# Performance work log

Hardware: AMD Instinct MI355X
Metric: run time of the kernel (lower is better)

## Reference

```python
import jax, jax.numpy as jnp
import numpy as np

B = 131072

def _lin(x, w, b):
    return x @ w.T + b

def setup_inputs() -> dict:
    key = jax.random.key(0)
    ks = jax.random.split(key, 32)
    def rn(k, shape, scale=0.05):
        return jax.random.normal(k, shape, dtype=jnp.float32) * scale
    inp = {
        "x": rn(ks[0], (B, 256), 1.0),
        "w": rn(ks[1], (B, 36), 1.0),
        "h0": rn(ks[2], (B, 32), 1.0),
        "c0": rn(ks[3], (B, 32), 1.0),
        "fc1_w": rn(ks[4], (128, 256)), "fc1_b": rn(ks[5], (128,)),
        "fc1a_w": rn(ks[6], (128, 164)), "fc1a_b": rn(ks[7], (128,)),
        "fc1b_w": rn(ks[8], (128, 128)), "fc1b_b": rn(ks[9], (128,)),
        "w_game": rn(ks[10], (1, 12), 1.0),
        "fc1c_w": rn(ks[11], (64, 140)), "fc1c_b": rn(ks[12], (64,)),
        "fc2_w": rn(ks[13], (32, 64)), "fc2_b": rn(ks[14], (32,)),
        "fc3_w": rn(ks[15], (32, 32)), "fc3_b": rn(ks[16], (32,)),
        "w_ih": rn(ks[17], (128, 32)), "w_hh": rn(ks[18], (128, 32)),
        "b_ih": rn(ks[19], (128,)), "b_hh": rn(ks[20], (128,)),
        "fc4_w": rn(ks[21], (32, 32)), "fc4_b": rn(ks[22], (32,)),
        "fc5_w": rn(ks[23], (1, 32)), "fc5_b": rn(ks[24], (1,)),
    }
    return inp

def reference(x, w, h0, c0, fc1_w, fc1_b, fc1a_w, fc1a_b, fc1b_w, fc1b_b,
              w_game, fc1c_w, fc1c_b, fc2_w, fc2_b, fc3_w, fc3_b,
              w_ih, w_hh, b_ih, b_hh, fc4_w, fc4_b, fc5_w, fc5_b):
    b = x.shape[0]
    h = jax.nn.relu(_lin(x, fc1_w, fc1_b))                      # [B,128]
    h = jnp.concatenate([h, w], axis=-1)                        # [B,164]
    h = jax.nn.relu(_lin(h, fc1a_w, fc1a_b))                    # [B,128]
    h = jax.nn.relu(_lin(h, fc1b_w, fc1b_b))                    # [B,128]
    wg = jnp.broadcast_to(w_game.reshape(1, 12), (b, 12))
    h = jnp.concatenate([h, wg], axis=-1)                       # [B,140]
    h = jax.nn.relu(_lin(h, fc1c_w, fc1c_b))                    # [B,64]
    h = jax.nn.relu(_lin(h, fc2_w, fc2_b))                      # [B,32]
    h = jax.nn.relu(_lin(h, fc3_w, fc3_b))                      # [B,32]
    # LSTMCell step (torch gate order: input, forget, cell, output)
    gates = _lin(h, w_ih, b_ih) + _lin(h0, w_hh, b_hh)          # [B,128]
    i_g, f_g, g_g, o_g = jnp.split(gates, 4, axis=-1)
    c_new = jax.nn.sigmoid(f_g) * c0 + jax.nn.sigmoid(i_g) * jnp.tanh(g_g)
    h_new = jax.nn.sigmoid(o_g) * jnp.tanh(c_new)               # [B,32]
    out = jax.nn.relu(_lin(h_new, fc4_w, fc4_b))                # [B,32]
    out = _lin(out, fc5_w, fc5_b)                               # [B,1]
    return jax.nn.sigmoid(out)
```

## Files before the change

kernel.cpp:

```cpp
#include <hip/hip_runtime.h>
#include <hip/hip_bf16.h>


typedef __bf16 bf16x8 __attribute__((ext_vector_type(8)));
typedef float  f32x4  __attribute__((ext_vector_type(4)));
typedef int    i32x4  __attribute__((ext_vector_type(4)));

#define MFMA16(A, B, C) __builtin_amdgcn_mfma_f32_16x16x32_bf16((A), (B), (C), 0, 0, 0)

#define WOFF_FC1A_H 0
#define WOFF_FC1B   16384
#define WOFF_FC1C   32768
#define LDS_ELEMS   40960
#define WOFF_FC1    40960
#define WOFF_FC1A_W 73728
#define WOFF_FC2    81920
#define WOFF_FC3    83968
#define WOFF_WIH    84992
#define WOFF_WHH    89088
#define WOFF_FC4    93184
#define WTOT        94208
#define BOFF_FC1  0
#define BOFF_FC1A 128
#define BOFF_FC1B 256
#define BOFF_FC1C 384
#define BOFF_FC2  448
#define BOFF_FC3  480
#define BOFF_LSTM 512
#define BOFF_FC4  640
#define BTOT      672

__device__ __forceinline__ void conv_frag(int rel, const float* __restrict__ src,
                                          __bf16* __restrict__ dst,
                                          int ns, int Krow, int kbase, int klim, int perm) {
    int j    = rel & 7;
    int lane = (rel >> 3) & 63;
    int fs   = rel >> 9;
    int s    = fs % ns;
    int t    = fs / ns;
    int gq   = lane >> 4;
    int n    = 16 * t + (lane & 15);
    int k    = perm ? (16 * (2 * s + (j >> 2)) + 4 * gq + (j & 3))
                    : (32 * s + 8 * gq + j);
    float v  = (k < klim) ? src[n * Krow + kbase + k] : 0.f;
    dst[rel] = (__bf16)v;
}

__global__ void prep_kernel(const float* __restrict__ fc1w,  const float* __restrict__ fc1b,
                            const float* __restrict__ fc1aw, const float* __restrict__ fc1ab,
                            const float* __restrict__ fc1bw, const float* __restrict__ fc1bb,
                            const float* __restrict__ wgame, const float* __restrict__ fc1cw,
                            const float* __restrict__ fc1cb, const float* __restrict__ fc2w,
                            const float* __restrict__ fc2b,  const float* __restrict__ fc3w,
                            const float* __restrict__ fc3b,  const float* __restrict__ wih,
                            const float* __restrict__ whh,   const float* __restrict__ bih,
                            const float* __restrict__ bhh,   const float* __restrict__ fc4w,
                            const float* __restrict__ fc4b,
                            __bf16* __restrict__ wsw, float* __restrict__ wsb) {
    int idx = blockIdx.x * 256 + threadIdx.x;
    if (idx < WTOT) {
        if      (idx < WOFF_FC1B)   conv_frag(idx - WOFF_FC1A_H, fc1aw, wsw + WOFF_FC1A_H, 4, 164,   0, 128, 1);
        else if (idx < WOFF_FC1C)   conv_frag(idx - WOFF_FC1B,   fc1bw, wsw + WOFF_FC1B,   4, 128,   0, 128, 1);
        else if (idx < WOFF_FC1)    conv_frag(idx - WOFF_FC1C,   fc1cw, wsw + WOFF_FC1C,   4, 140,   0, 128, 1);
        else if (idx < WOFF_FC1A_W) conv_frag(idx - WOFF_FC1,    fc1w,  wsw + WOFF_FC1,    8, 256,   0, 256, 0);
        else if (idx < WOFF_FC2)    conv_frag(idx - WOFF_FC1A_W, fc1aw, wsw + WOFF_FC1A_W, 2, 164, 128,  36, 0);
        else if (idx < WOFF_FC3)    conv_frag(idx - WOFF_FC2,    fc2w,  wsw + WOFF_FC2,    2,  64,   0,  64, 1);
        else if (idx < WOFF_WIH)    conv_frag(idx - WOFF_FC3,    fc3w,  wsw + WOFF_FC3,    1,  32,   0,  32, 1);
        else if (idx < WOFF_WHH)    conv_frag(idx - WOFF_WIH,    wih,   wsw + WOFF_WIH,    1,  32,   0,  32, 1);
        else if (idx < WOFF_FC4)    conv_frag(idx - WOFF_WHH,    whh,   wsw + WOFF_WHH,    1,  32,   0,  32, 0);
        else                        conv_frag(idx - WOFF_FC4,    fc4w,  wsw + WOFF_FC4,    1,  32,   0,  32, 1);
    } else if (idx < WTOT + BTOT) {
        int bi = idx - WTOT;
        float v;
        if      (bi < 128) v = fc1b[bi];
        else if (bi < 256) v = fc1ab[bi - 128];
        else if (bi < 384) v = fc1bb[bi - 256];
        else if (bi < 448) {
            int n = bi - 384;
            v = fc1cb[n];
            for (int q = 0; q < 12; ++q) v += fc1cw[n * 140 + 128 + q] * wgame[q];
        }
        else if (bi < 480) v = fc2b[bi - 448];
        else if (bi < 512) v = fc3b[bi - 480];
        else if (bi < 640) { int n = bi - 512; v = bih[n] + bhh[n]; }
        else               v = fc4b[bi - 640];
        wsb[bi] = v;
    }
}

__device__ __forceinline__ bf16x8 ld8f(const float* __restrict__ p) {
    f32x4 a = *(const f32x4*)p;
    f32x4 b = *(const f32x4*)(p + 4);
    bf16x8 r;
    r[0] = (__bf16)a[0]; r[1] = (__bf16)a[1]; r[2] = (__bf16)a[2]; r[3] = (__bf16)a[3];
    r[4] = (__bf16)b[0]; r[5] = (__bf16)b[1]; r[6] = (__bf16)b[2]; r[7] = (__bf16)b[3];
    return r;
}

__device__ __forceinline__ bf16x8 ld4f_masked(const float* __restrict__ p, bool on) {
    f32x4 v = {0.f, 0.f, 0.f, 0.f};
    if (on) v = *(const f32x4*)p;
    bf16x8 r;
    r[0] = (__bf16)v[0]; r[1] = (__bf16)v[1]; r[2] = (__bf16)v[2]; r[3] = (__bf16)v[3];
    r[4] = (__bf16)0.f;  r[5] = (__bf16)0.f;  r[6] = (__bf16)0.f;  r[7] = (__bf16)0.f;
    return r;
}

__device__ __forceinline__ bf16x8 packrelu(const f32x4* a, int s) {
    bf16x8 r;
#pragma unroll
    for (int j = 0; j < 8; ++j) {
        float v = a[2 * s + (j >> 2)][j & 3];
        r[j] = (__bf16)fmaxf(v, 0.f);
    }
    return r;
}

__device__ __forceinline__ float sigm(float v)  { return 1.f / (1.f + __expf(-v)); }
__device__ __forceinline__ float tanh_(float v) { return 1.f - 2.f / (1.f + __expf(2.f * v)); }

__global__ __launch_bounds__(512, 4) void fused_mlp_lstm(
        const float* __restrict__ x,  const float* __restrict__ w,
        const float* __restrict__ h0, const float* __restrict__ c0,
        const float* __restrict__ fc5w, const float* __restrict__ fc5b,
        const __bf16* __restrict__ wsw, const float* __restrict__ wsb,
        float* __restrict__ out) {
    __shared__ __align__(16) __bf16 slds[LDS_ELEMS];

    const int tid     = threadIdx.x;
    const int lane    = tid & 63;
    const int gq      = lane >> 4;
    const int mr      = lane & 15;
    const int rowbase = blockIdx.x * 128 + (tid >> 6) * 16;
    const int row     = rowbase + mr;

    {
        const i32x4* gs = (const i32x4*)wsw;
        i32x4*       sd = (i32x4*)slds;
#pragma unroll
        for (int i = 0; i < 10; ++i) sd[i * 512 + tid] = gs[i * 512 + tid];
    }

    const bf16x8* Gfc1  = (const bf16x8*)(wsw + WOFF_FC1);
    const bf16x8* Wf1aH = (const bf16x8*)(slds + WOFF_FC1A_H);
    const bf16x8* Wfc1b = (const bf16x8*)(slds + WOFF_FC1B);
    const bf16x8* Wfc1c = (const bf16x8*)(slds + WOFF_FC1C);
    const bf16x8* Wf1aW = (const bf16x8*)(wsw + WOFF_FC1A_W);
    const bf16x8* Wfc2  = (const bf16x8*)(wsw + WOFF_FC2);
    const bf16x8* Wfc3  = (const bf16x8*)(wsw + WOFF_FC3);
    const bf16x8* Wwih  = (const bf16x8*)(wsw + WOFF_WIH);
    const bf16x8* Wwhh  = (const bf16x8*)(wsw + WOFF_WHH);
    const bf16x8* Wfc4  = (const bf16x8*)(wsw + WOFF_FC4);

    bf16x8 h1f[4];
    {
        f32x4 acc1[8];
#pragma unroll
        for (int t = 0; t < 8; ++t)
            acc1[t] = *(const f32x4*)(wsb + BOFF_FC1 + 16 * t + 4 * gq);
        const float* xrow = x + row * 256 + 8 * gq;
#pragma unroll
        for (int p = 0; p < 4; ++p) {
            bf16x8 a0 = ld8f(xrow + 64 * p);
            bf16x8 a1 = ld8f(xrow + 64 * p + 32);
#pragma unroll
            for (int t = 0; t < 8; ++t)
                acc1[t] = MFMA16(Gfc1[(t * 8 + 2 * p) * 64 + lane], a0, acc1[t]);
#pragma unroll
            for (int t = 0; t < 8; ++t)
                acc1[t] = MFMA16(Gfc1[(t * 8 + 2 * p + 1) * 64 + lane], a1, acc1[t]);
        }
#pragma unroll
        for (int s = 0; s < 4; ++s) h1f[s] = packrelu(acc1, s);
    }

    __syncthreads();

    bf16x8 h2f[4];
    {
        bf16x8 wxa0 = ld8f(w + row * 36 + 8 * gq);
        bf16x8 wxa1 = ld4f_masked(w + row * 36 + 32, gq == 0);
        f32x4 acc2[8];
#pragma unroll
        for (int t = 0; t < 8; ++t)
            acc2[t] = *(const f32x4*)(wsb + BOFF_FC1A + 16 * t + 4 * gq);
#pragma unroll
        for (int s = 0; s < 4; ++s)
#pragma unroll
            for (int t = 0; t < 8; ++t)
                acc2[t] = MFMA16(Wf1aH[(t * 4 + s) * 64 + lane], h1f[s], acc2[t]);
#pragma unroll
        for (int t = 0; t < 8; ++t) {
            acc2[t] = MFMA16(Wf1aW[(t * 2 + 0) * 64 + lane], wxa0, acc2[t]);
            acc2[t] = MFMA16(Wf1aW[(t * 2 + 1) * 64 + lane], wxa1, acc2[t]);
        }
#pragma unroll
        for (int s = 0; s < 4; ++s) h2f[s] = packrelu(acc2, s);
    }

    bf16x8 h3f[4];
    {
        f32x4 acc3[8];
#pragma unroll
        for (int t = 0; t < 8; ++t)
            acc3[t] = *(const f32x4*)(wsb + BOFF_FC1B + 16 * t + 4 * gq);
#pragma unroll
        for (int s = 0; s < 4; ++s)
#pragma unroll
            for (int t = 0; t < 8; ++t)
                acc3[t] = MFMA16(Wfc1b[(t * 4 + s) * 64 + lane], h2f[s], acc3[t]);
#pragma unroll
        for (int s = 0; s < 4; ++s) h3f[s] = packrelu(acc3, s);
    }

    bf16x8 h0f  = ld8f(h0 + row * 32 + 8 * gq);
    f32x4  c0r0 = *(const f32x4*)(c0 + row * 32 + 4 * gq);
    f32x4  c0r1 = *(const f32x4*)(c0 + row * 32 + 16 + 4 * gq);

    bf16x8 h4f[2];
    {
        f32x4 acc4[4];
#pragma unroll
        for (int t = 0; t < 4; ++t)
            acc4[t] = *(const f32x4*)(wsb + BOFF_FC1C + 16 * t + 4 * gq);
#pragma unroll
        for (int s = 0; s < 4; ++s)
#pragma unroll
            for (int t = 0; t < 4; ++t)
                acc4[t] = MFMA16(Wfc1c[(t * 4 + s) * 64 + lane], h3f[s], acc4[t]);
#pragma unroll
        for (int s = 0; s < 2; ++s) h4f[s] = packrelu(acc4, s);
    }

    bf16x8 h5f;
    {
        f32x4 acc5[2];
#pragma unroll
        for (int t = 0; t < 2; ++t)
            acc5[t] = *(const f32x4*)(wsb + BOFF_FC2 + 16 * t + 4 * gq);
#pragma unroll
        for (int s = 0; s < 2; ++s)
#pragma unroll
            for (int t = 0; t < 2; ++t)
                acc5[t] = MFMA16(Wfc2[(t * 2 + s) * 64 + lane], h4f[s], acc5[t]);
        h5f = packrelu(acc5, 0);
    }

    bf16x8 h6f;
    {
        f32x4 acc6[2];
#pragma unroll
        for (int t = 0; t < 2; ++t)
            acc6[t] = *(const f32x4*)(wsb + BOFF_FC3 + 16 * t + 4 * gq);
#pragma unroll
        for (int t = 0; t < 2; ++t)
            acc6[t] = MFMA16(Wfc3[t * 64 + lane], h5f, acc6[t]);
        h6f = packrelu(acc6, 0);
    }

    bf16x8 hnf;
    {
        f32x4 accg[8];
#pragma unroll
        for (int t = 0; t < 8; ++t)
            accg[t] = *(const f32x4*)(wsb + BOFF_LSTM + 16 * t + 4 * gq);
#pragma unroll
        for (int t = 0; t < 8; ++t)
            accg[t] = MFMA16(Wwih[t * 64 + lane], h6f, accg[t]);
#pragma unroll
        for (int t = 0; t < 8; ++t)
            accg[t] = MFMA16(Wwhh[t * 64 + lane], h0f, accg[t]);
#pragma unroll
        for (int t2 = 0; t2 < 2; ++t2) {
            f32x4 cc = t2 ? c0r1 : c0r0;
#pragma unroll
            for (int r = 0; r < 4; ++r) {
                float ig = accg[t2][r];
                float fg = accg[2 + t2][r];
                float gg = accg[4 + t2][r];
                float og = accg[6 + t2][r];
                float cn = sigm(fg) * cc[r] + sigm(ig) * tanh_(gg);
                hnf[t2 * 4 + r] = (__bf16)(sigm(og) * tanh_(cn));
            }
        }
    }

    f32x4 acco[2];
#pragma unroll
    for (int t = 0; t < 2; ++t)
        acco[t] = *(const f32x4*)(wsb + BOFF_FC4 + 16 * t + 4 * gq);
#pragma unroll
    for (int t = 0; t < 2; ++t)
        acco[t] = MFMA16(Wfc4[t * 64 + lane], hnf, acco[t]);

    f32x4 w5a = *(const f32x4*)(fc5w + 4 * gq);
    f32x4 w5b = *(const f32x4*)(fc5w + 16 + 4 * gq);
    float p = 0.f;
#pragma unroll
    for (int r = 0; r < 4; ++r) {
        p += fmaxf(acco[0][r], 0.f) * w5a[r];
        p += fmaxf(acco[1][r], 0.f) * w5b[r];
    }
    p += __shfl_xor(p, 16);
    p += __shfl_xor(p, 32);
    float res = sigm(p + fc5b[0]);
    if (lane < 16) out[rowbase + lane] = res;
}

extern "C" void kernel_launch(void* const* d_in, const int* in_sizes, int n_in,
                              void* d_out, int out_size, void* d_ws, size_t ws_size,
                              hipStream_t stream) {
    const float* x     = (const float*)d_in[0];
    const float* w     = (const float*)d_in[1];
    const float* h0    = (const float*)d_in[2];
    const float* c0    = (const float*)d_in[3];
    const float* fc1w  = (const float*)d_in[4];
    const float* fc1b  = (const float*)d_in[5];
    const float* fc1aw = (const float*)d_in[6];
    const float* fc1ab = (const float*)d_in[7];
    const float* fc1bw = (const float*)d_in[8];
    const float* fc1bb = (const float*)d_in[9];
    const float* wgame = (const float*)d_in[10];
    const float* fc1cw = (const float*)d_in[11];
    const float* fc1cb = (const float*)d_in[12];
    const float* fc2w  = (const float*)d_in[13];
    const float* fc2b  = (const float*)d_in[14];
    const float* fc3w  = (const float*)d_in[15];
    const float* fc3b  = (const float*)d_in[16];
    const float* wih   = (const float*)d_in[17];
    const float* whh   = (const float*)d_in[18];
    const float* bih   = (const float*)d_in[19];
    const float* bhh   = (const float*)d_in[20];
    const float* fc4w  = (const float*)d_in[21];
    const float* fc4b  = (const float*)d_in[22];
    const float* fc5w  = (const float*)d_in[23];
    const float* fc5b  = (const float*)d_in[24];

    __bf16* wsw = (__bf16*)d_ws;
    float*  wsb = (float*)((char*)d_ws + WTOT * sizeof(__bf16));
    (void)ws_size; (void)n_in; (void)out_size;

    const int Btot = in_sizes[0] / 256;

    prep_kernel<<<(WTOT + BTOT + 255) / 256, 256, 0, stream>>>(
        fc1w, fc1b, fc1aw, fc1ab, fc1bw, fc1bb, wgame, fc1cw, fc1cb,
        fc2w, fc2b, fc3w, fc3b, wih, whh, bih, bhh, fc4w, fc4b, wsw, wsb);

    fused_mlp_lstm<<<Btot / 128, 512, 0, stream>>>(
        x, w, h0, c0, fc5w, fc5b, wsw, wsb, (float*)d_out);
}
```

Measured before the change: 76.74 us.

## Split output features across waves and stage activations in LDS instead of weights

The big layers (fc1, fc1a, fc1b, fc1c) are restructured so each wave owns a slice of output features across all 128 block rows. Each wave keeps its weight fragments in registers, and activations are exchanged through LDS in MFMA fragment layout. Before, each wave computed every output feature for its own 16 rows and streamed all weights from LDS or global memory. This cuts per-wave weight traffic and shrinks LDS use from 80KB to 48KB, which may allow more resident blocks. The cost is several extra block-wide barriers and LDS activation round-trips per layer.

```diff
diff --git a/kernel.cpp b/kernel.cpp
--- a/kernel.cpp
+++ b/kernel.cpp
@@ -3,15 +3,14 @@
 
 
 typedef __bf16 bf16x8 __attribute__((ext_vector_type(8)));
+typedef __bf16 bf16x4 __attribute__((ext_vector_type(4)));
 typedef float  f32x4  __attribute__((ext_vector_type(4)));
-typedef int    i32x4  __attribute__((ext_vector_type(4)));
 
 #define MFMA16(A, B, C) __builtin_amdgcn_mfma_f32_16x16x32_bf16((A), (B), (C), 0, 0, 0)
 
 #define WOFF_FC1A_H 0
 #define WOFF_FC1B   16384
 #define WOFF_FC1C   32768
-#define LDS_ELEMS   40960
 #define WOFF_FC1    40960
 #define WOFF_FC1A_W 73728
 #define WOFF_FC2    81920
@@ -29,6 +28,14 @@
 #define BOFF_LSTM 512
 #define BOFF_FC4  640
 #define BTOT      672
+
+#define ACT_ELEMS 16384
+#define WLDS_BASE 16384
+#define LDS_TOT   24576
+
+__device__ __forceinline__ int actoff(int s2, int m, int lane) {
+    return ((s2 * 8 + m) * 64 + lane) * 8;
+}
 
 __device__ __forceinline__ void conv_frag(int rel, const float* __restrict__ src,
                                           __bf16* __restrict__ dst,
@@ -116,6 +123,13 @@
     return r;
 }
 
+__device__ __forceinline__ bf16x4 pack4(f32x4 a) {
+    bf16x4 r;
+#pragma unroll
+    for (int j = 0; j < 4; ++j) r[j] = (__bf16)fmaxf(a[j], 0.f);
+    return r;
+}
+
 __device__ __forceinline__ float sigm(float v)  { return 1.f / (1.f + __expf(-v)); }
 __device__ __forceinline__ float tanh_(float v) { return 1.f - 2.f / (1.f + __expf(2.f * v)); }
 
@@ -125,186 +139,230 @@
         const float* __restrict__ fc5w, const float* __restrict__ fc5b,
         const __bf16* __restrict__ wsw, const float* __restrict__ wsb,
         float* __restrict__ out) {
-    __shared__ __align__(16) __bf16 slds[LDS_ELEMS];
-
-    const int tid     = threadIdx.x;
-    const int lane    = tid & 63;
-    const int gq      = lane >> 4;
-    const int mr      = lane & 15;
-    const int rowbase = blockIdx.x * 128 + (tid >> 6) * 16;
-    const int row     = rowbase + mr;
+    __shared__ __align__(16) __bf16 slds[LDS_TOT];
+
+    const int tid  = threadIdx.x;
+    const int lane = tid & 63;
+    const int wv   = tid >> 6;
+    const int gq   = lane >> 4;
+    const int mr   = lane & 15;
+    const int blkrow = blockIdx.x * 128;
+
+#pragma unroll
+    for (int pass = 0; pass < 2; ++pass) {
+        int fid  = pass * 8 + wv;
+        int m    = fid & 7;
+        int wrow = blkrow + 16 * m + mr;
+        bf16x8 v = (pass == 0) ? ld8f(w + wrow * 36 + 8 * gq)
+                               : ld4f_masked(w + wrow * 36 + 32, gq == 0);
+        *(bf16x8*)(slds + WLDS_BASE + (fid * 64 + lane) * 8) = v;
+    }
 
     {
-        const i32x4* gs = (const i32x4*)wsw;
-        i32x4*       sd = (i32x4*)slds;
-#pragma unroll
-        for (int i = 0; i < 10; ++i) sd[i * 512 + tid] = gs[i * 512 + tid];
-    }
-
-    const bf16x8* Gfc1  = (const bf16x8*)(wsw + WOFF_FC1);
-    const bf16x8* Wf1aH = (const bf16x8*)(slds + WOFF_FC1A_H);
-    const bf16x8* Wfc1b = (const bf16x8*)(slds + WOFF_FC1B);
-    const bf16x8* Wfc1c = (const bf16x8*)(slds + WOFF_FC1C);
-    const bf16x8* Wf1aW = (const bf16x8*)(wsw + WOFF_FC1A_W);
-    const bf16x8* Wfc2  = (const bf16x8*)(wsw + WOFF_FC2);
-    const bf16x8* Wfc3  = (const bf16x8*)(wsw + WOFF_FC3);
-    const bf16x8* Wwih  = (const bf16x8*)(wsw + WOFF_WIH);
-    const bf16x8* Wwhh  = (const bf16x8*)(wsw + WOFF_WHH);
-    const bf16x8* Wfc4  = (const bf16x8*)(wsw + WOFF_FC4);
-
-    bf16x8 h1f[4];
+        const int p  = wv & 3;
+        const int th = wv >> 2;
+        const int row0 = blkrow + 32 * p + mr;
+        const int row1 = row0 + 16;
+        const bf16x8* Gfc1 = (const bf16x8*)(wsw + WOFF_FC1);
+
+        f32x4 accA[4], accB[4];
+#pragma unroll
+        for (int tt = 0; tt < 4; ++tt) {
+            f32x4 bv = *(const f32x4*)(wsb + BOFF_FC1 + 16 * (4 * th + tt) + 4 * gq);
+            accA[tt] = bv; accB[tt] = bv;
+        }
+#pragma unroll
+        for (int s = 0; s < 8; ++s) {
+            bf16x8 xa = ld8f(x + row0 * 256 + 32 * s + 8 * gq);
+            bf16x8 xb = ld8f(x + row1 * 256 + 32 * s + 8 * gq);
+#pragma unroll
+            for (int tt = 0; tt < 4; ++tt) {
+                bf16x8 wf = Gfc1[((4 * th + tt) * 8 + s) * 64 + lane];
+                accA[tt] = MFMA16(wf, xa, accA[tt]);
+                accB[tt] = MFMA16(wf, xb, accB[tt]);
+            }
+        }
+#pragma unroll
+        for (int sh = 0; sh < 2; ++sh) {
+            *(bf16x8*)(slds + actoff(2 * th + sh, 2 * p + 0, lane)) = packrelu(accA, sh);
+            *(bf16x8*)(slds + actoff(2 * th + sh, 2 * p + 1, lane)) = packrelu(accB, sh);
+        }
+    }
+    __syncthreads();
+
     {
-        f32x4 acc1[8];
-#pragma unroll
-        for (int t = 0; t < 8; ++t)
-            acc1[t] = *(const f32x4*)(wsb + BOFF_FC1 + 16 * t + 4 * gq);
-        const float* xrow = x + row * 256 + 8 * gq;
-#pragma unroll
-        for (int p = 0; p < 4; ++p) {
-            bf16x8 a0 = ld8f(xrow + 64 * p);
-            bf16x8 a1 = ld8f(xrow + 64 * p + 32);
+        const bf16x8* GA = (const bf16x8*)(wsw + WOFF_FC1A_H);
+        const bf16x8* GW = (const bf16x8*)(wsw + WOFF_FC1A_W);
+        bf16x8 WA[4], WW[2];
+#pragma unroll
+        for (int s = 0; s < 4; ++s) WA[s] = GA[(wv * 4 + s) * 64 + lane];
+#pragma unroll
+        for (int s = 0; s < 2; ++s) WW[s] = GW[(wv * 2 + s) * 64 + lane];
+
+        f32x4 acc[8];
+        f32x4 bv = *(const f32x4*)(wsb + BOFF_FC1A + 16 * wv + 4 * gq);
+#pragma unroll
+        for (int m = 0; m < 8; ++m) acc[m] = bv;
+#pragma unroll
+        for (int s = 0; s < 4; ++s)
+#pragma unroll
+            for (int m = 0; m < 8; ++m) {
+                bf16x8 af = *(const bf16x8*)(slds + actoff(s, m, lane));
+                acc[m] = MFMA16(WA[s], af, acc[m]);
+            }
+#pragma unroll
+        for (int s2 = 0; s2 < 2; ++s2)
+#pragma unroll
+            for (int m = 0; m < 8; ++m) {
+                bf16x8 af = *(const bf16x8*)(slds + WLDS_BASE + ((s2 * 8 + m) * 64 + lane) * 8);
+                acc[m] = MFMA16(WW[s2], af, acc[m]);
+            }
+        __syncthreads();
+        const int jh = wv & 1, s2o = wv >> 1;
+#pragma unroll
+        for (int m = 0; m < 8; ++m)
+            *(bf16x4*)(slds + actoff(s2o, m, lane) + jh * 4) = pack4(acc[m]);
+    }
+    __syncthreads();
+
+    {
+        const bf16x8* GB = (const bf16x8*)(wsw + WOFF_FC1B);
+        bf16x8 WB[4];
+#pragma unroll
+        for (int s = 0; s < 4; ++s) WB[s] = GB[(wv * 4 + s) * 64 + lane];
+
+        f32x4 acc[8];
+        f32x4 bv = *(const f32x4*)(wsb + BOFF_FC1B + 16 * wv + 4 * gq);
+#pragma unroll
+        for (int m = 0; m < 8; ++m) acc[m] = bv;
+#pragma unroll
+        for (int s = 0; s < 4; ++s)
+#pragma unroll
+            for (int m = 0; m < 8; ++m) {
+                bf16x8 af = *(const bf16x8*)(slds + actoff(s, m, lane));
+                acc[m] = MFMA16(WB[s], af, acc[m]);
+            }
+        __syncthreads();
+        const int jh = wv & 1, s2o = wv >> 1;
+#pragma unroll
+        for (int m = 0; m < 8; ++m)
+            *(bf16x4*)(slds + actoff(s2o, m, lane) + jh * 4) = pack4(acc[m]);
+    }
+    __syncthreads();
+
+    {
+        const bf16x8* GC = (const bf16x8*)(wsw + WOFF_FC1C);
+        const int tc = wv & 3, hh = wv >> 2;
+        bf16x8 WC[4];
+#pragma unroll
+        for (int s = 0; s < 4; ++s) WC[s] = GC[(tc * 4 + s) * 64 + lane];
+
+        f32x4 acc4[4];
+        f32x4 bv = *(const f32x4*)(wsb + BOFF_FC1C + 16 * tc + 4 * gq);
+#pragma unroll
+        for (int mi = 0; mi < 4; ++mi) acc4[mi] = bv;
+#pragma unroll
+        for (int s = 0; s < 4; ++s)
+#pragma unroll
+            for (int mi = 0; mi < 4; ++mi) {
+                bf16x8 af = *(const bf16x8*)(slds + actoff(s, 4 * hh + mi, lane));
+                acc4[mi] = MFMA16(WC[s], af, acc4[mi]);
+            }
+        __syncthreads();
+        const int jh = tc & 1, s2o = tc >> 1;
+#pragma unroll
+        for (int mi = 0; mi < 4; ++mi)
+            *(bf16x4*)(slds + actoff(s2o, 4 * hh + mi, lane) + jh * 4) = pack4(acc4[mi]);
+    }
+    __syncthreads();
+
+    {
+        const int rowbase = blkrow + 16 * wv;
+        const int row     = rowbase + mr;
+        const bf16x8* Wfc2 = (const bf16x8*)(wsw + WOFF_FC2);
+        const bf16x8* Wfc3 = (const bf16x8*)(wsw + WOFF_FC3);
+        const bf16x8* Wwih = (const bf16x8*)(wsw + WOFF_WIH);
+        const bf16x8* Wwhh = (const bf16x8*)(wsw + WOFF_WHH);
+        const bf16x8* Wfc4 = (const bf16x8*)(wsw + WOFF_FC4);
+
+        bf16x8 h4f[2];
+        h4f[0] = *(const bf16x8*)(slds + actoff(0, wv, lane));
+        h4f[1] = *(const bf16x8*)(slds + actoff(1, wv, lane));
+
+        bf16x8 h0f  = ld8f(h0 + row * 32 + 8 * gq);
+        f32x4  c0r0 = *(const f32x4*)(c0 + row * 32 + 4 * gq);
+        f32x4  c0r1 = *(const f32x4*)(c0 + row * 32 + 16 + 4 * gq);
+
+        bf16x8 h5f;
+        {
+            f32x4 acc5[2];
+#pragma unroll
+            for (int t = 0; t < 2; ++t)
+                acc5[t] = *(const f32x4*)(wsb + BOFF_FC2 + 16 * t + 4 * gq);
+#pragma unroll
+            for (int s = 0; s < 2; ++s)
+#pragma unroll
+                for (int t = 0; t < 2; ++t)
+                    acc5[t] = MFMA16(Wfc2[(t * 2 + s) * 64 + lane], h4f[s], acc5[t]);
+            h5f = packrelu(acc5, 0);
+        }
+        bf16x8 h6f;
+        {
+            f32x4 acc6[2];
+#pragma unroll
+            for (int t = 0; t < 2; ++t)
+                acc6[t] = *(const f32x4*)(wsb + BOFF_FC3 + 16 * t + 4 * gq);
+#pragma unroll
+            for (int t = 0; t < 2; ++t)
+                acc6[t] = MFMA16(Wfc3[t * 64 + lane], h5f, acc6[t]);
+            h6f = packrelu(acc6, 0);
+        }
+        bf16x8 hnf;
+        {
+            f32x4 accg[8];
 #pragma unroll
             for (int t = 0; t < 8; ++t)
-                acc1[t] = MFMA16(Gfc1[(t * 8 + 2 * p) * 64 + lane], a0, acc1[t]);
+                accg[t] = *(const f32x4*)(wsb + BOFF_LSTM + 16 * t + 4 * gq);
 #pragma unroll
             for (int t = 0; t < 8; ++t)
-                acc1[t] = MFMA16(Gfc1[(t * 8 + 2 * p + 1) * 64 + lane], a1, acc1[t]);
-        }
-#pragma unroll
-        for (int s = 0; s < 4; ++s) h1f[s] = packrelu(acc1, s);
-    }
-
-    __syncthreads();
-
-    bf16x8 h2f[4];
-    {
-        bf16x8 wxa0 = ld8f(w + row * 36 + 8 * gq);
-        bf16x8 wxa1 = ld4f_masked(w + row * 36 + 32, gq == 0);
-        f32x4 acc2[8];
-#pragma unroll
-        for (int t = 0; t < 8; ++t)
-            acc2[t] = *(const f32x4*)(wsb + BOFF_FC1A + 16 * t + 4 * gq);
-#pragma unroll
-        for (int s = 0; s < 4; ++s)
+                accg[t] = MFMA16(Wwih[t * 64 + lane], h6f, accg[t]);
 #pragma unroll
             for (int t = 0; t < 8; ++t)
-                acc2[t] = MFMA16(Wf1aH[(t * 4 + s) * 64 + lane], h1f[s], acc2[t]);
-#pragma unroll
-        for (int t = 0; t < 8; ++t) {
-            acc2[t] = MFMA16(Wf1aW[(t * 2 + 0) * 64 + lane], wxa0, acc2[t]);
-            acc2[t] = MFMA16(Wf1aW[(t * 2 + 1) * 64 + lane], wxa1, acc2[t]);
-        }
-#pragma unroll
-        for (int s = 0; s < 4; ++s) h2f[s] = packrelu(acc2, s);
-    }
-
-    bf16x8 h3f[4];
-    {
-        f32x4 acc3[8];
-#pragma unroll
-        for (int t = 0; t < 8; ++t)
-            acc3[t] = *(const f32x4*)(wsb + BOFF_FC1B + 16 * t + 4 * gq);
-#pragma unroll
-        for (int s = 0; s < 4; ++s)
-#pragma unroll
-            for (int t = 0; t < 8; ++t)
-                acc3[t] = MFMA16(Wfc1b[(t * 4 + s) * 64 + lane], h2f[s], acc3[t]);
-#pragma unroll
-        for (int s = 0; s < 4; ++s) h3f[s] = packrelu(acc3, s);
-    }
-
-    bf16x8 h0f  = ld8f(h0 + row * 32 + 8 * gq);
-    f32x4  c0r0 = *(const f32x4*)(c0 + row * 32 + 4 * gq);
-    f32x4  c0r1 = *(const f32x4*)(c0 + row * 32 + 16 + 4 * gq);
-
-    bf16x8 h4f[2];
-    {
-        f32x4 acc4[4];
-#pragma unroll
-        for (int t = 0; t < 4; ++t)
-            acc4[t] = *(const f32x4*)(wsb + BOFF_FC1C + 16 * t + 4 * gq);
-#pragma unroll
-        for (int s = 0; s < 4; ++s)
-#pragma unroll
-            for (int t = 0; t < 4; ++t)
-                acc4[t] = MFMA16(Wfc1c[(t * 4 + s) * 64 + lane], h3f[s], acc4[t]);
-#pragma unroll
-        for (int s = 0; s < 2; ++s) h4f[s] = packrelu(acc4, s);
-    }
-
-    bf16x8 h5f;
-    {
-        f32x4 acc5[2];
+                accg[t] = MFMA16(Wwhh[t * 64 + lane], h0f, accg[t]);
+#pragma unroll
+            for (int t2 = 0; t2 < 2; ++t2) {
+                f32x4 cc = t2 ? c0r1 : c0r0;
+#pragma unroll
+                for (int r = 0; r < 4; ++r) {
+                    float ig = accg[t2][r];
+                    float fg = accg[2 + t2][r];
+                    float gg = accg[4 + t2][r];
+                    float og = accg[6 + t2][r];
+                    float cn = sigm(fg) * cc[r] + sigm(ig) * tanh_(gg);
+                    hnf[t2 * 4 + r] = (__bf16)(sigm(og) * tanh_(cn));
+                }
+            }
+        }
+        f32x4 acco[2];
 #pragma unroll
         for (int t = 0; t < 2; ++t)
-            acc5[t] = *(const f32x4*)(wsb + BOFF_FC2 + 16 * t + 4 * gq);
-#pragma unroll
-        for (int s = 0; s < 2; ++s)
-#pragma unroll
-            for (int t = 0; t < 2; ++t)
-                acc5[t] = MFMA16(Wfc2[(t * 2 + s) * 64 + lane], h4f[s], acc5[t]);
-        h5f = packrelu(acc5, 0);
-    }
-
-    bf16x8 h6f;
-    {
-        f32x4 acc6[2];
+            acco[t] = *(const f32x4*)(wsb + BOFF_FC4 + 16 * t + 4 * gq);
 #pragma unroll
         for (int t = 0; t < 2; ++t)
-            acc6[t] = *(const f32x4*)(wsb + BOFF_FC3 + 16 * t + 4 * gq);
-#pragma unroll
-        for (int t = 0; t < 2; ++t)
-            acc6[t] = MFMA16(Wfc3[t * 64 + lane], h5f, acc6[t]);
-        h6f = packrelu(acc6, 0);
-    }
-
-    bf16x8 hnf;
-    {
-        f32x4 accg[8];
-#pragma unroll
-        for (int t = 0; t < 8; ++t)
-            accg[t] = *(const f32x4*)(wsb + BOFF_LSTM + 16 * t + 4 * gq);
-#pragma unroll
-        for (int t = 0; t < 8; ++t)
-            accg[t] = MFMA16(Wwih[t * 64 + lane], h6f, accg[t]);
-#pragma unroll
-        for (int t = 0; t < 8; ++t)
-            accg[t] = MFMA16(Wwhh[t * 64 + lane], h0f, accg[t]);
-#pragma unroll
-        for (int t2 = 0; t2 < 2; ++t2) {
-            f32x4 cc = t2 ? c0r1 : c0r0;
-#pragma unroll
-            for (int r = 0; r < 4; ++r) {
-                float ig = accg[t2][r];
-                float fg = accg[2 + t2][r];
-                float gg = accg[4 + t2][r];
-                float og = accg[6 + t2][r];
-                float cn = sigm(fg) * cc[r] + sigm(ig) * tanh_(gg);
-                hnf[t2 * 4 + r] = (__bf16)(sigm(og) * tanh_(cn));
-            }
-        }
-    }
-
-    f32x4 acco[2];
-#pragma unroll
-    for (int t = 0; t < 2; ++t)
-        acco[t] = *(const f32x4*)(wsb + BOFF_FC4 + 16 * t + 4 * gq);
-#pragma unroll
-    for (int t = 0; t < 2; ++t)
-        acco[t] = MFMA16(Wfc4[t * 64 + lane], hnf, acco[t]);
-
-    f32x4 w5a = *(const f32x4*)(fc5w + 4 * gq);
-    f32x4 w5b = *(const f32x4*)(fc5w + 16 + 4 * gq);
-    float p = 0.f;
-#pragma unroll
-    for (int r = 0; r < 4; ++r) {
-        p += fmaxf(acco[0][r], 0.f) * w5a[r];
-        p += fmaxf(acco[1][r], 0.f) * w5b[r];
-    }
-    p += __shfl_xor(p, 16);
-    p += __shfl_xor(p, 32);
-    float res = sigm(p + fc5b[0]);
-    if (lane < 16) out[rowbase + lane] = res;
+            acco[t] = MFMA16(Wfc4[t * 64 + lane], hnf, acco[t]);
+        f32x4 w5a = *(const f32x4*)(fc5w + 4 * gq);
+        f32x4 w5b = *(const f32x4*)(fc5w + 16 + 4 * gq);
+        float p = 0.f;
+#pragma unroll
+        for (int r = 0; r < 4; ++r) {
+            p += fmaxf(acco[0][r], 0.f) * w5a[r];
+            p += fmaxf(acco[1][r], 0.f) * w5b[r];
+        }
+        p += __shfl_xor(p, 16);
+        p += __shfl_xor(p, 32);
+        float res = sigm(p + fc5b[0]);
+        if (lane < 16) out[rowbase + lane] = res;
+    }
 }
 
 extern "C" void kernel_launch(void* const* d_in, const int* in_sizes, int n_in,
```

After: 78.37 us. +2.1%, slower.
